# Kernel tuning notes

Hardware: AMD Instinct MI355X
Metric: run time of the kernel (lower is better)

Reference implementation:

```python
import jax, jax.numpy as jnp
import numpy as np

L, H, E, V, BS = 12, 12, 768, 50257, 1024  # layers, heads, n_embd, vocab, block_size
B, T = 2, 1024
D = E // H


def setup_inputs() -> dict:
    key = jax.random.key(0)
    ks = jax.random.split(key, 10)
    s = 0.02
    d = {}
    d["idx"] = jax.random.randint(ks[0], (B, T), 0, V)
    d["targets"] = jax.random.randint(ks[1], (B, T), 0, V)
    # embeddings (wte tied with lm_head)
    d["wte"] = (jax.random.normal(ks[2], (V, E)) * s).astype(jnp.float32)
    d["wpe"] = (jax.random.normal(ks[3], (BS, E)) * s).astype(jnp.float32)
    # stacked per-layer params; Linear weights stored [in, out] (= torch W.T)
    d["ln1_w"] = jnp.ones((L, E), jnp.float32)
    d["ln1_b"] = jnp.zeros((L, E), jnp.float32)
    d["attn_w"] = (jax.random.normal(ks[4], (L, E, 3 * E)) * s).astype(jnp.float32)
    d["attn_b"] = jnp.zeros((L, 3 * E), jnp.float32)
    d["proj_w"] = (jax.random.normal(ks[5], (L, E, E)) * s).astype(jnp.float32)
    d["proj_b"] = jnp.zeros((L, E), jnp.float32)
    d["ln2_w"] = jnp.ones((L, E), jnp.float32)
    d["ln2_b"] = jnp.zeros((L, E), jnp.float32)
    d["fc_w"] = (jax.random.normal(ks[6], (L, E, 4 * E)) * s).astype(jnp.float32)
    d["fc_b"] = jnp.zeros((L, 4 * E), jnp.float32)
    d["fcproj_w"] = (jax.random.normal(ks[7], (L, 4 * E, E)) * s).astype(jnp.float32)
    d["fcproj_b"] = jnp.zeros((L, E), jnp.float32)
    d["lnf_w"] = jnp.ones((E,), jnp.float32)
    d["lnf_b"] = jnp.zeros((E,), jnp.float32)
    return d


def _ln(x, w, b, eps=1e-5):
    m = jnp.mean(x, -1, keepdims=True)
    v = jnp.mean(jnp.square(x - m), -1, keepdims=True)
    return (x - m) * jax.lax.rsqrt(v + eps) * w + b


def _block(x, p, mask):
    l1w, l1b, aw, ab, pw, pb, l2w, l2b, fw, fb, fpw, fpb = p
    Bx, Tx, C = x.shape
    # causal self-attention (explicit QK^T + mask + softmax + AV, as in source)
    qkv = _ln(x, l1w, l1b) @ aw + ab                       # [B,T,3E]
    q, k, v = jnp.split(qkv, 3, axis=-1)
    q = q.reshape(Bx, Tx, H, D).transpose(0, 2, 1, 3)       # [B,H,T,D]
    k = k.reshape(Bx, Tx, H, D).transpose(0, 2, 1, 3)
    v = v.reshape(Bx, Tx, H, D).transpose(0, 2, 1, 3)
    att = jnp.einsum('bhqd,bhkd->bhqk', q, k) * (1.0 / np.sqrt(D))
    att = jnp.where(mask, att, -jnp.inf)
    att = jax.nn.softmax(att, axis=-1)
    y = jnp.einsum('bhqk,bhkd->bhqd', att, v)
    y = y.transpose(0, 2, 1, 3).reshape(Bx, Tx, C)
    x = x + y @ pw + pb
    # MLP with tanh-approx GELU
    h = jax.nn.gelu(_ln(x, l2w, l2b) @ fw + fb, approximate=True)
    x = x + h @ fpw + fpb
    return x


def reference(idx, targets, wte, wpe, ln1_w, ln1_b, attn_w, attn_b, proj_w, proj_b,
              ln2_w, ln2_b, fc_w, fc_b, fcproj_w, fcproj_b, lnf_w, lnf_b):
    Tq = idx.shape[1]
    x = wte[idx] + wpe[:Tq]                                 # [B,T,E]
    mask = jnp.tril(jnp.ones((Tq, Tq), dtype=bool))

    def step(x, p):
        return _block(x, p, mask), None

    layer_params = (ln1_w, ln1_b, attn_w, attn_b, proj_w, proj_b,
                    ln2_w, ln2_b, fc_w, fc_b, fcproj_w, fcproj_b)
    x, _ = jax.lax.scan(step, x, layer_params)
    x = _ln(x, lnf_w, lnf_b)
    logits = x @ wte.T                                      # tied lm_head, [B,T,V]
    logp = jax.nn.log_softmax(logits, axis=-1)
    nll = -jnp.take_along_axis(logp, targets[..., None], axis=-1)[..., 0]
    loss = jnp.mean(nll)
    return logits, loss
```

## Files before the change

### kernel.cpp

```cpp
#include <hip/hip_runtime.h>
#include <hip/hip_bf16.h>
#include <math.h>

#define LNUM 12
#define HNUM 12
#define EDIM 768
#define VDIM 50257
#define BDIM 2
#define TDIM 1024
#define BT (BDIM*TDIM)
#define E3 (3*EDIM)
#define E4 (4*EDIM)
#define NPB (2*((VDIM+127)/128))

typedef __bf16 bf16x8 __attribute__((ext_vector_type(8)));
typedef __bf16 bf16x4 __attribute__((ext_vector_type(4)));
typedef float f32x4 __attribute__((ext_vector_type(4)));

__device__ __forceinline__ float gelu_f(float x) {
    float u = 0.7978845608028654f * (x + 0.044715f * x * x * x);
    return 0.5f * x * (1.0f + tanhf(u));
}

__device__ __forceinline__ void gl16(const void* g, void* l) {
    __builtin_amdgcn_global_load_lds(
        (const __attribute__((address_space(1))) unsigned int*)g,
        (__attribute__((address_space(3))) unsigned int*)l,
        16, 0, 0);
}

__global__ __launch_bounds__(256) void embed_kernel(
    const int* __restrict__ idx, const float* __restrict__ wte,
    const float* __restrict__ wpe, float* __restrict__ x)
{
    const int row = blockIdx.x;
    const int t = row % TDIM;
    const int tok = idx[row];
    const float* we = wte + (size_t)tok * EDIM;
    const float* pe = wpe + (size_t)t * EDIM;
    float* xr = x + (size_t)row * EDIM;
    for (int e = threadIdx.x; e < EDIM; e += 256) xr[e] = we[e] + pe[e];
}

__global__ __launch_bounds__(256) void ln_kernel(
    const float* __restrict__ in, const float* __restrict__ w,
    const float* __restrict__ b, __bf16* __restrict__ out)
{
    const int row = blockIdx.x * 4 + (threadIdx.x >> 6);
    const int lane = threadIdx.x & 63;
    const float4* xr = (const float4*)(in + (size_t)row * EDIM);
    float4 a0 = xr[lane], a1 = xr[64 + lane], a2 = xr[128 + lane];
    float s = a0.x + a0.y + a0.z + a0.w + a1.x + a1.y + a1.z + a1.w
            + a2.x + a2.y + a2.z + a2.w;
    #pragma unroll
    for (int off = 32; off; off >>= 1) s += __shfl_xor(s, off);
    const float mean = s * (1.0f / EDIM);
    float4 d0 = make_float4(a0.x - mean, a0.y - mean, a0.z - mean, a0.w - mean);
    float4 d1 = make_float4(a1.x - mean, a1.y - mean, a1.z - mean, a1.w - mean);
    float4 d2 = make_float4(a2.x - mean, a2.y - mean, a2.z - mean, a2.w - mean);
    float v = d0.x*d0.x + d0.y*d0.y + d0.z*d0.z + d0.w*d0.w
            + d1.x*d1.x + d1.y*d1.y + d1.z*d1.z + d1.w*d1.w
            + d2.x*d2.x + d2.y*d2.y + d2.z*d2.z + d2.w*d2.w;
    #pragma unroll
    for (int off = 32; off; off >>= 1) v += __shfl_xor(v, off);
    const float inv = rsqrtf(v * (1.0f / EDIM) + 1e-5f);
    const float4* w4 = (const float4*)w;
    const float4* b4 = (const float4*)b;
    __bf16* orow = out + (size_t)row * EDIM;
    #pragma unroll
    for (int c = 0; c < 3; ++c) {
        float4 dd = c == 0 ? d0 : (c == 1 ? d1 : d2);
        float4 ww = w4[c * 64 + lane], bb = b4[c * 64 + lane];
        bf16x4 o;
        o[0] = (__bf16)(dd.x * inv * ww.x + bb.x);
        o[1] = (__bf16)(dd.y * inv * ww.y + bb.y);
        o[2] = (__bf16)(dd.z * inv * ww.z + bb.z);
        o[3] = (__bf16)(dd.w * inv * ww.w + bb.w);
        *(bf16x4*)(orow + c * 256 + lane * 4) = o;
    }
}

__global__ __launch_bounds__(256) void convt_kernel(
    const float* __restrict__ in, __bf16* __restrict__ out, int K, int N)
{
    in  += (size_t)blockIdx.z * K * N;
    out += (size_t)blockIdx.z * K * N;
    __shared__ float t[32][33];
    const int n0 = blockIdx.x * 32, k0 = blockIdx.y * 32;
    const int r = threadIdx.x >> 3, c = (threadIdx.x & 7) * 4;
    float4 v = *(const float4*)(in + (size_t)(k0 + r) * N + n0 + c);
    t[r][c + 0] = v.x; t[r][c + 1] = v.y; t[r][c + 2] = v.z; t[r][c + 3] = v.w;
    __syncthreads();
    bf16x4 o;
    o[0] = (__bf16)t[c + 0][r];
    o[1] = (__bf16)t[c + 1][r];
    o[2] = (__bf16)t[c + 2][r];
    o[3] = (__bf16)t[c + 3][r];
    *(bf16x4*)(out + (size_t)(n0 + r) * K + k0 + c) = o;
}

__global__ __launch_bounds__(256) void cvt_kernel(
    const float* __restrict__ in, __bf16* __restrict__ out, long n4)
{
    for (long i = blockIdx.x * 256L + threadIdx.x; i < n4; i += (long)gridDim.x * 256L) {
        float4 v = ((const float4*)in)[i];
        out[i * 4 + 0] = (__bf16)v.x;
        out[i * 4 + 1] = (__bf16)v.y;
        out[i * 4 + 2] = (__bf16)v.z;
        out[i * 4 + 3] = (__bf16)v.w;
    }
}

template<int BM, int BN, int BK, bool BIAS, bool GELU_, bool RES_, bool OUTBF, bool NGUARD, bool LOGITS>
__global__ __launch_bounds__(256, 2) void mgemm(
    const __bf16* __restrict__ A, const __bf16* __restrict__ Bt,
    const float* __restrict__ bias, const float* __restrict__ res,
    void* __restrict__ Cout, float* __restrict__ part, int M, int N, int K)
{
    constexpr int WM = BM / 2, WN = BN / 2;
    constexpr int FM = WM / 16, FN = WN / 16;
    constexpr int KS = BK / 32;
    constexpr int TBA = BM * BK * 2;
    constexpr int TBB = BN * BK * 2;
    constexpr int rA = TBA / 4096, rB = TBB / 4096;
    constexpr int RPI = 2048 / BK;
    constexpr int CPR = BK / 8;
    __shared__ __align__(16) __bf16 As[3 * BM * BK];
    __shared__ __align__(16) __bf16 Bs[3 * BN * BK];
    const int tid = threadIdx.x;
    const int lane = tid & 63;
    const int wave = tid >> 6;
    const int wr = wave >> 1, wc = wave & 1;

    int bm, bn;
    if (LOGITS) {
        const int wg = blockIdx.x;
        bm = (wg >> 3) & 7;
        bn = (wg & 7) + ((wg >> 6) << 3);
        if (bn * BN >= N) return;
    } else { bm = blockIdx.y; bn = blockIdx.x; }
    const int m0 = bm * BM;
    const int n0 = bn * BN;

    const int srow = tid / CPR;
    const int skey = (BK == 32) ? ((srow >> 1) & 3) : (srow & 7);
    const int c0 = (tid % CPR) ^ skey;

    const __bf16* gA = A + (size_t)(m0 + srow) * K + c0 * 8;
    const __bf16* gB[rB];
    #pragma unroll
    for (int r = 0; r < rB; ++r) {
        int nr = n0 + srow + r * RPI;
        if (NGUARD) nr = nr < N ? nr : N - 1;
        gB[r] = Bt + (size_t)nr * K + c0 * 8;
    }

    const int fr = lane & 15;
    const int g = lane >> 4;
    const int fkey = (BK == 32) ? ((fr >> 1) & 3) : (fr & 7);

    f32x4 acc[FM][FN];
    #pragma unroll
    for (int i = 0; i < FM; i++)
        #pragma unroll
        for (int j = 0; j < FN; j++) acc[i][j] = (f32x4){0.f, 0.f, 0.f, 0.f};

    const int nt = K / BK;

    auto stage = [&](int kk, int b) {
        #pragma unroll
        for (int r = 0; r < rA; ++r)
            gl16(gA + (size_t)r * RPI * K + kk, (char*)As + b * TBA + r * 4096 + tid * 16);
        #pragma unroll
        for (int r = 0; r < rB; ++r)
            gl16(gB[r] + kk, (char*)Bs + b * TBB + r * 4096 + tid * 16);
    };

    stage(0, 0);
    if (nt > 1) stage(BK, 1);

    int b0 = 0, b1 = 1, b2 = 2;
    for (int t = 0; t < nt; ++t) {
        if (t + 1 < nt) {
            static_assert(rA + rB == 4 || rA + rB == 6, "vmcnt literal");
            if constexpr (rA + rB == 4) asm volatile("s_waitcnt vmcnt(4)" ::: "memory");
            else                        asm volatile("s_waitcnt vmcnt(6)" ::: "memory");
        } else {
            asm volatile("s_waitcnt vmcnt(0)" ::: "memory");
        }
        asm volatile("s_barrier" ::: "memory");
        if (t + 2 < nt) stage((t + 2) * BK, b2);

        const char* pa = (const char*)As + b0 * TBA;
        const char* pb = (const char*)Bs + b0 * TBB;
        bf16x8 af[FM][KS], bfr[FN][KS];
        #pragma unroll
        for (int i = 0; i < FM; i++)
            #pragma unroll
            for (int kc = 0; kc < KS; kc++)
                af[i][kc] = *(const bf16x8*)(pa + (wr * WM + i * 16 + fr) * (2 * BK)
                                                + (((kc * 4 + g) ^ fkey) << 4));
        #pragma unroll
        for (int j = 0; j < FN; j++)
            #pragma unroll
            for (int kc = 0; kc < KS; kc++)
                bfr[j][kc] = *(const bf16x8*)(pb + (wc * WN + j * 16 + fr) * (2 * BK)
                                                 + (((kc * 4 + g) ^ fkey) << 4));
        #pragma unroll
        for (int kc = 0; kc < KS; kc++)
            #pragma unroll
            for (int i = 0; i < FM; i++)
                #pragma unroll
                for (int j = 0; j < FN; j++)
                    acc[i][j] = __builtin_amdgcn_mfma_f32_16x16x32_bf16(af[i][kc], bfr[j][kc], acc[i][j], 0, 0, 0);
        const int tmp = b0; b0 = b1; b1 = b2; b2 = tmp;
    }

    const int crow = g * 4;
    if constexpr (LOGITS) {
        constexpr int NH = WN / 64;
        const int cg0 = bn * (BN / 64) + wc * NH;
        #pragma unroll
        for (int i = 0; i < FM; i++) {
            #pragma unroll
            for (int r = 0; r < 4; r++) {
                const int m = m0 + wr * WM + i * 16 + crow + r;
                float se[NH];
                #pragma unroll
                for (int h = 0; h < NH; h++) se[h] = 0.f;
                #pragma unroll
                for (int j = 0; j < FN; j++) {
                    const int n = n0 + wc * WN + j * 16 + fr;
                    if (n < N) {
                        float v = acc[i][j][r];
                        ((float*)Cout)[(size_t)m * N + n] = v;
                        se[j >> 2] += __expf(v);
                    }
                }
                #pragma unroll
                for (int h = 0; h < NH; h++) {
                    float sh = se[h];
                    sh += __shfl_xor(sh, 1); sh += __shfl_xor(sh, 2);
                    sh += __shfl_xor(sh, 4); sh += __shfl_xor(sh, 8);
                    if (fr == 0 && (n0 + wc * WN + h * 64) < N)
                        part[(size_t)m * NPB + cg0 + h] = sh;
                }
            }
        }
    } else {
        #pragma unroll
        for (int i = 0; i < FM; i++) {
            #pragma unroll
            for (int r = 0; r < 4; r++) {
                const int m = m0 + wr * WM + i * 16 + crow + r;
                #pragma unroll
                for (int j = 0; j < FN; j++) {
                    const int n = n0 + wc * WN + j * 16 + fr;
                    if (!NGUARD || n < N) {
                        float v = acc[i][j][r];
                        if (BIAS) v += bias[n];
                        if (GELU_) v = gelu_f(v);
                        if (RES_) v += res[(size_t)m * N + n];
                        if (OUTBF) ((__bf16*)Cout)[(size_t)m * N + n] = (__bf16)v;
                        else       ((float*)Cout)[(size_t)m * N + n] = v;
                    }
                }
            }
        }
    }
}

__global__ __launch_bounds__(128) void fattn_kernel(
    const __bf16* __restrict__ qkv, __bf16* __restrict__ y)
{
    const int bq = gridDim.x - 1 - blockIdx.x;
    const int h = blockIdx.y, b = blockIdx.z;
    const int tid = threadIdx.x, lane = tid & 63, w = tid >> 6;
    const int fr = lane & 15, g = lane >> 4;

    __shared__ __align__(16) __bf16 Ks[64 * 64];
    __shared__ __align__(16) __bf16 Vt[64 * 64];
    __shared__ __align__(16) __bf16 Ps[2][16 * 64];

    const __bf16* base = qkv + (size_t)b * TDIM * E3;
    const int q0w = bq * 32 + w * 16;
    const int NT = (bq >> 1) + 1;
    const int last = NT - 1;

    bf16x8 qf[2];
    {
        const __bf16* qp = base + (size_t)(q0w + fr) * E3 + h * 64 + g * 8;
        qf[0] = *(const bf16x8*)qp;
        qf[1] = *(const bf16x8*)(qp + 32);
    }

    const int r0 = tid >> 3, ch = tid & 7;
    bf16x8 kr[4], vr[4];

    #pragma unroll
    for (int it = 0; it < 4; ++it) {
        const int row = it * 16 + r0;
        const __bf16* gp = base + (size_t)row * E3 + EDIM + h * 64 + ch * 8;
        kr[it] = *(const bf16x8*)gp;
        vr[it] = *(const bf16x8*)(gp + EDIM);
    }
    #pragma unroll
    for (int it = 0; it < 4; ++it) {
        const int row = it * 16 + r0;
        *(bf16x8*)(Ks + row * 64 + ((ch ^ (row & 7)) << 3)) = kr[it];
        #pragma unroll
        for (int j = 0; j < 8; ++j) {
            const int d = ch * 8 + j;
            const int key = ((d >> 3) ^ d) & 7;
            Vt[d * 64 + ((((row >> 3) ^ key) << 3) + (row & 7))] = vr[it][j];
        }
    }
    __syncthreads();

    float m[4] = {-1e30f, -1e30f, -1e30f, -1e30f};
    float l[4] = {0.f, 0.f, 0.f, 0.f};
    f32x4 acc[4];
    #pragma unroll
    for (int jd = 0; jd < 4; ++jd) acc[jd] = (f32x4){0.f, 0.f, 0.f, 0.f};

    for (int kt = 0; kt < NT; ++kt) {
        if (kt < last) {
            const int k1 = (kt + 1) * 64;
            #pragma unroll
            for (int it = 0; it < 4; ++it) {
                const int row = it * 16 + r0;
                const __bf16* gp = base + (size_t)(k1 + row) * E3 + EDIM + h * 64 + ch * 8;
                kr[it] = *(const bf16x8*)gp;
                vr[it] = *(const bf16x8*)(gp + EDIM);
            }
        }

        const int k0 = kt * 64;
        f32x4 s[4];
        #pragma unroll
        for (int jf = 0; jf < 4; ++jf) {
            const int krow = jf * 16 + fr;
            f32x4 sv = (f32x4){0.f, 0.f, 0.f, 0.f};
            #pragma unroll
            for (int kc = 0; kc < 2; ++kc) {
                bf16x8 kf = *(const bf16x8*)(Ks + krow * 64 + (((kc * 4 + g) ^ (fr & 7)) << 3));
                sv = __builtin_amdgcn_mfma_f32_16x16x32_bf16(qf[kc], kf, sv, 0, 0, 0);
            }
            s[jf] = sv;
        }
        #pragma unroll
        for (int jf = 0; jf < 4; ++jf)
            #pragma unroll
            for (int r = 0; r < 4; ++r) s[jf][r] *= 0.125f;
        if (kt == last) {
            #pragma unroll
            for (int jf = 0; jf < 4; ++jf) {
                const int k = k0 + jf * 16 + fr;
                #pragma unroll
                for (int r = 0; r < 4; ++r) {
                    const int q = q0w + g * 4 + r;
                    if (k > q) s[jf][r] = -1e30f;
                }
            }
        }

        #pragma unroll
        for (int r = 0; r < 4; ++r) {
            float mx = fmaxf(fmaxf(s[0][r], s[1][r]), fmaxf(s[2][r], s[3][r]));
            mx = fmaxf(mx, __shfl_xor(mx, 1));
            mx = fmaxf(mx, __shfl_xor(mx, 2));
            mx = fmaxf(mx, __shfl_xor(mx, 4));
            mx = fmaxf(mx, __shfl_xor(mx, 8));
            const float mn = fmaxf(m[r], mx);
            const float sc2 = __expf(m[r] - mn);
            m[r] = mn;
            float rs = 0.f;
            #pragma unroll
            for (int jf = 0; jf < 4; ++jf) {
                const float p = __expf(s[jf][r] - mn);
                s[jf][r] = p;
                rs += p;
            }
            rs += __shfl_xor(rs, 1);
            rs += __shfl_xor(rs, 2);
            rs += __shfl_xor(rs, 4);
            rs += __shfl_xor(rs, 8);
            l[r] = l[r] * sc2 + rs;
            #pragma unroll
            for (int jd = 0; jd < 4; ++jd) acc[jd][r] *= sc2;
        }

        __bf16* pw = &Ps[w][0];
        #pragma unroll
        for (int jf = 0; jf < 4; ++jf) {
            const int chp = jf * 2 + (fr >> 3);
            #pragma unroll
            for (int r = 0; r < 4; ++r) {
                const int row = g * 4 + r;
                pw[row * 64 + (((chp ^ (row & 7)) << 3) + (fr & 7))] = (__bf16)s[jf][r];
            }
        }
        asm volatile("s_waitcnt lgkmcnt(0)" ::: "memory");
        bf16x8 pa[2];
        #pragma unroll
        for (int kc = 0; kc < 2; ++kc)
            pa[kc] = *(const bf16x8*)(pw + fr * 64 + (((kc * 4 + g) ^ (fr & 7)) << 3));

        #pragma unroll
        for (int jd = 0; jd < 4; ++jd) {
            const int d = jd * 16 + fr;
            const int key = ((d >> 3) ^ d) & 7;
            #pragma unroll
            for (int kc = 0; kc < 2; ++kc) {
                bf16x8 vf = *(const bf16x8*)(Vt + d * 64 + (((kc * 4 + g) ^ key) << 3));
                acc[jd] = __builtin_amdgcn_mfma_f32_16x16x32_bf16(pa[kc], vf, acc[jd], 0, 0, 0);
            }
        }

        if (kt < last) {
            __syncthreads();
            #pragma unroll
            for (int it = 0; it < 4; ++it) {
                const int row = it * 16 + r0;
                *(bf16x8*)(Ks + row * 64 + ((ch ^ (row & 7)) << 3)) = kr[it];
                #pragma unroll
                for (int j = 0; j < 8; ++j) {
                    const int d = ch * 8 + j;
                    const int key = ((d >> 3) ^ d) & 7;
                    Vt[d * 64 + ((((row >> 3) ^ key) << 3) + (row & 7))] = vr[it][j];
                }
            }
            __syncthreads();
        }
    }

    #pragma unroll
    for (int r = 0; r < 4; ++r) {
        const float inv = 1.0f / l[r];
        const int q = q0w + g * 4 + r;
        __bf16* yp = y + ((size_t)(b * TDIM + q)) * EDIM + h * 64;
        #pragma unroll
        for (int jd = 0; jd < 4; ++jd)
            yp[jd * 16 + fr] = (__bf16)(acc[jd][r] * inv);
    }
}

__global__ __launch_bounds__(256) void lsefin_kernel(
    const float* __restrict__ part, const float* __restrict__ logits,
    const int* __restrict__ targets, float* __restrict__ rr)
{
    const int row = blockIdx.x, tid = threadIdx.x;
    float s = 0.f;
    for (int j = tid; j < NPB; j += 256) s += part[(size_t)row * NPB + j];
    #pragma unroll
    for (int off = 32; off; off >>= 1) s += __shfl_xor(s, off);
    __shared__ float red[4];
    if ((tid & 63) == 0) red[tid >> 6] = s;
    __syncthreads();
    if (tid == 0) {
        float S = red[0] + red[1] + red[2] + red[3];
        rr[row] = logf(S) - logits[(size_t)row * VDIM + targets[row]];
    }
}

__global__ __launch_bounds__(256) void loss_reduce_kernel(
    const float* __restrict__ rr, float* __restrict__ out)
{
    const int tid = threadIdx.x;
    float s = 0.f;
    for (int i = tid; i < BT; i += 256) s += rr[i];
    #pragma unroll
    for (int off = 32; off; off >>= 1) s += __shfl_xor(s, off);
    __shared__ float red[4];
    if ((tid & 63) == 0) red[tid >> 6] = s;
    __syncthreads();
    if (tid == 0) out[0] = (red[0] + red[1] + red[2] + red[3]) * (1.0f / BT);
}

extern "C" void kernel_launch(void* const* d_in, const int* in_sizes, int n_in,
                              void* d_out, int out_size, void* d_ws, size_t ws_size,
                              hipStream_t stream)
{
    const int*   idx     = (const int*)d_in[0];
    const int*   targets = (const int*)d_in[1];
    const float* wte     = (const float*)d_in[2];
    const float* wpe     = (const float*)d_in[3];
    const float* ln1_w   = (const float*)d_in[4];
    const float* ln1_b   = (const float*)d_in[5];
    const float* attn_w  = (const float*)d_in[6];
    const float* attn_b  = (const float*)d_in[7];
    const float* proj_w  = (const float*)d_in[8];
    const float* proj_b  = (const float*)d_in[9];
    const float* ln2_w   = (const float*)d_in[10];
    const float* ln2_b   = (const float*)d_in[11];
    const float* fc_w    = (const float*)d_in[12];
    const float* fc_b    = (const float*)d_in[13];
    const float* fcp_w   = (const float*)d_in[14];
    const float* fcp_b   = (const float*)d_in[15];
    const float* lnf_w   = (const float*)d_in[16];
    const float* lnf_b   = (const float*)d_in[17];

    float* logits = (float*)d_out;

    const size_t slq = (size_t)EDIM * E3, slp = (size_t)EDIM * EDIM;
    const size_t slf = (size_t)EDIM * E4, slfp = (size_t)E4 * EDIM;

    char* wp = (char*)d_ws;
    float*  x     = (float*)wp;   wp += (size_t)BT * EDIM * 4;
    __bf16* qkvb  = (__bf16*)wp;  wp += (size_t)BT * E3 * 2;
    __bf16* xnbf  = (__bf16*)wp;  wp += (size_t)BT * EDIM * 2;
    __bf16* ybf   = (__bf16*)wp;  wp += (size_t)BT * EDIM * 2;
    __bf16* hbf   = (__bf16*)wp;  wp += (size_t)BT * E4 * 2;
    __bf16* wteb  = (__bf16*)wp;  wp += (size_t)VDIM * EDIM * 2;
    float*  part  = (float*)wp;   wp += (size_t)BT * NPB * 4;
    float*  rr    = (float*)wp;   wp += (size_t)BT * 4;
    __bf16* wqkvb = (__bf16*)wp;

    const size_t wbytes_all = (slq + slp + slf + slfp) * 2 * LNUM;
    const size_t used = (size_t)(wp - (char*)d_ws);
    const bool big = ws_size >= used + wbytes_all;
    const size_t L = big ? LNUM : 1;
    __bf16* wprjb = wqkvb + slq * L;
    __bf16* wfcb  = wprjb + slp * L;
    __bf16* wfpb  = wfcb  + slf * L;

    embed_kernel<<<BT, 256, 0, stream>>>(idx, wte, wpe, x);
    cvt_kernel<<<2048, 256, 0, stream>>>(wte, wteb, (long)VDIM * EDIM / 4);

    if (big) {
        convt_kernel<<<dim3(E3 / 32, EDIM / 32, LNUM), 256, 0, stream>>>(attn_w, wqkvb, EDIM, E3);
        convt_kernel<<<dim3(EDIM / 32, EDIM / 32, LNUM), 256, 0, stream>>>(proj_w, wprjb, EDIM, EDIM);
        convt_kernel<<<dim3(E4 / 32, EDIM / 32, LNUM), 256, 0, stream>>>(fc_w, wfcb, EDIM, E4);
        convt_kernel<<<dim3(EDIM / 32, E4 / 32, LNUM), 256, 0, stream>>>(fcp_w, wfpb, E4, EDIM);
    }

    for (int l = 0; l < LNUM; ++l) {
        const __bf16* wq = wqkvb + (big ? (size_t)l * slq : 0);
        const __bf16* wpj = wprjb + (big ? (size_t)l * slp : 0);
        const __bf16* wf = wfcb + (big ? (size_t)l * slf : 0);
        const __bf16* wfp = wfpb + (big ? (size_t)l * slfp : 0);

        ln_kernel<<<BT / 4, 256, 0, stream>>>(x, ln1_w + (size_t)l * EDIM,
                                              ln1_b + (size_t)l * EDIM, xnbf);
        if (!big)
            convt_kernel<<<dim3(E3 / 32, EDIM / 32), 256, 0, stream>>>(
                attn_w + (size_t)l * slq, (__bf16*)wq, EDIM, E3);
        mgemm<64, 64, 64, true, false, false, true, false, false>
            <<<dim3(E3 / 64, BT / 64), 256, 0, stream>>>(
            xnbf, wq, attn_b + (size_t)l * E3, nullptr, qkvb, nullptr, BT, E3, EDIM);
        fattn_kernel<<<dim3(TDIM / 32, HNUM, BDIM), 128, 0, stream>>>(qkvb, ybf);
        if (!big)
            convt_kernel<<<dim3(EDIM / 32, EDIM / 32), 256, 0, stream>>>(
                proj_w + (size_t)l * slp, (__bf16*)wpj, EDIM, EDIM);
        mgemm<64, 64, 64, true, false, true, false, false, false>
            <<<dim3(EDIM / 64, BT / 64), 256, 0, stream>>>(
            ybf, wpj, proj_b + (size_t)l * EDIM, x, x, nullptr, BT, EDIM, EDIM);
        ln_kernel<<<BT / 4, 256, 0, stream>>>(x, ln2_w + (size_t)l * EDIM,
                                              ln2_b + (size_t)l * EDIM, xnbf);
        if (!big)
            convt_kernel<<<dim3(E4 / 32, EDIM / 32), 256, 0, stream>>>(
                fc_w + (size_t)l * slf, (__bf16*)wf, EDIM, E4);
        mgemm<64, 64, 64, true, true, false, true, false, false>
            <<<dim3(E4 / 64, BT / 64), 256, 0, stream>>>(
            xnbf, wf, fc_b + (size_t)l * E4, nullptr, hbf, nullptr, BT, E4, EDIM);
        if (!big)
            convt_kernel<<<dim3(EDIM / 32, E4 / 32), 256, 0, stream>>>(
                fcp_w + (size_t)l * slfp, (__bf16*)wfp, E4, EDIM);
        mgemm<64, 64, 64, true, false, true, false, false, false>
            <<<dim3(EDIM / 64, BT / 64), 256, 0, stream>>>(
            hbf, wfp, fcp_b + (size_t)l * EDIM, x, x, nullptr, BT, EDIM, E4);
    }

    ln_kernel<<<BT / 4, 256, 0, stream>>>(x, lnf_w, lnf_b, xnbf);
    mgemm<256, 128, 32, false, false, false, false, true, true>
        <<<dim3(64 * 50), 256, 0, stream>>>(
        xnbf, wteb, nullptr, nullptr, logits, part, BT, VDIM, EDIM);
    lsefin_kernel<<<BT, 256, 0, stream>>>(part, logits, targets, rr);
    loss_reduce_kernel<<<1, 256, 0, stream>>>(rr, logits + (size_t)BT * VDIM);
}
```

Before: 2.139 ms.

## Split-K the projection GEMMs and fuse residual reduction with next LayerNorm

The two N=768 GEMMs (attention proj and MLP down-proj) now run as 2-way split-K launches that write fp32 partial sums. A new redln kernel adds both partials, the bias and the residual, updates x, and applies the following LayerNorm in one pass, so the separate LN launches go away. Attention MFMA sections are also wrapped in s_setprio raises. This gives the small-grid GEMMs more blocks to fill the GPU, at the cost of writing and reading an extra 2xBTxE fp32 partial buffer each time.

```diff
diff --git a/kernel.cpp b/kernel.cpp
--- a/kernel.cpp
+++ b/kernel.cpp
@@ -76,6 +76,55 @@
         o[1] = (__bf16)(dd.y * inv * ww.y + bb.y);
         o[2] = (__bf16)(dd.z * inv * ww.z + bb.z);
         o[3] = (__bf16)(dd.w * inv * ww.w + bb.w);
+        *(bf16x4*)(orow + c * 256 + lane * 4) = o;
+    }
+}
+
+__global__ __launch_bounds__(256) void redln_kernel(
+    const float* __restrict__ ps, const float* __restrict__ bias,
+    float* __restrict__ x, const float* __restrict__ w,
+    const float* __restrict__ b, __bf16* __restrict__ out)
+{
+    const int row = blockIdx.x * 4 + (threadIdx.x >> 6);
+    const int lane = threadIdx.x & 63;
+    const float4* p0 = (const float4*)(ps + (size_t)row * EDIM);
+    const float4* p1 = (const float4*)(ps + (size_t)(BT + row) * EDIM);
+    float4* xr = (float4*)(x + (size_t)row * EDIM);
+    const float4* b4 = (const float4*)bias;
+    float4 a[3];
+    #pragma unroll
+    for (int c = 0; c < 3; ++c) {
+        const int i = c * 64 + lane;
+        float4 u = p0[i], v = p1[i], xx = xr[i], bb = b4[i];
+        a[c] = make_float4(u.x + v.x + xx.x + bb.x, u.y + v.y + xx.y + bb.y,
+                           u.z + v.z + xx.z + bb.z, u.w + v.w + xx.w + bb.w);
+        xr[i] = a[c];
+    }
+    float s = a[0].x + a[0].y + a[0].z + a[0].w + a[1].x + a[1].y + a[1].z + a[1].w
+            + a[2].x + a[2].y + a[2].z + a[2].w;
+    #pragma unroll
+    for (int off = 32; off; off >>= 1) s += __shfl_xor(s, off);
+    const float mean = s * (1.0f / EDIM);
+    float v = 0.f;
+    #pragma unroll
+    for (int c = 0; c < 3; ++c) {
+        a[c] = make_float4(a[c].x - mean, a[c].y - mean, a[c].z - mean, a[c].w - mean);
+        v += a[c].x * a[c].x + a[c].y * a[c].y + a[c].z * a[c].z + a[c].w * a[c].w;
+    }
+    #pragma unroll
+    for (int off = 32; off; off >>= 1) v += __shfl_xor(v, off);
+    const float inv = rsqrtf(v * (1.0f / EDIM) + 1e-5f);
+    const float4* w4 = (const float4*)w;
+    const float4* lb4 = (const float4*)b;
+    __bf16* orow = out + (size_t)row * EDIM;
+    #pragma unroll
+    for (int c = 0; c < 3; ++c) {
+        float4 ww = w4[c * 64 + lane], bb = lb4[c * 64 + lane];
+        bf16x4 o;
+        o[0] = (__bf16)(a[c].x * inv * ww.x + bb.x);
+        o[1] = (__bf16)(a[c].y * inv * ww.y + bb.y);
+        o[2] = (__bf16)(a[c].z * inv * ww.z + bb.z);
+        o[3] = (__bf16)(a[c].w * inv * ww.w + bb.w);
         *(bf16x4*)(orow + c * 256 + lane * 4) = o;
     }
 }
@@ -115,7 +164,7 @@
 __global__ __launch_bounds__(256, 2) void mgemm(
     const __bf16* __restrict__ A, const __bf16* __restrict__ Bt,
     const float* __restrict__ bias, const float* __restrict__ res,
-    void* __restrict__ Cout, float* __restrict__ part, int M, int N, int K)
+    void* __restrict__ Cout, float* __restrict__ part, int M, int N, int K, int lda)
 {
     constexpr int WM = BM / 2, WN = BN / 2;
     constexpr int FM = WM / 16, FN = WN / 16;
@@ -141,18 +190,20 @@
     } else { bm = blockIdx.y; bn = blockIdx.x; }
     const int m0 = bm * BM;
     const int n0 = bn * BN;
+    const int kbase = blockIdx.z * K;
+    const size_t zoff = (size_t)blockIdx.z * M * N;
 
     const int srow = tid / CPR;
     const int skey = (BK == 32) ? ((srow >> 1) & 3) : (srow & 7);
     const int c0 = (tid % CPR) ^ skey;
 
-    const __bf16* gA = A + (size_t)(m0 + srow) * K + c0 * 8;
+    const __bf16* gA = A + (size_t)(m0 + srow) * lda + kbase + c0 * 8;
     const __bf16* gB[rB];
     #pragma unroll
     for (int r = 0; r < rB; ++r) {
         int nr = n0 + srow + r * RPI;
         if (NGUARD) nr = nr < N ? nr : N - 1;
-        gB[r] = Bt + (size_t)nr * K + c0 * 8;
+        gB[r] = Bt + (size_t)nr * lda + kbase + c0 * 8;
     }
 
     const int fr = lane & 15;
@@ -170,7 +221,7 @@
     auto stage = [&](int kk, int b) {
         #pragma unroll
         for (int r = 0; r < rA; ++r)
-            gl16(gA + (size_t)r * RPI * K + kk, (char*)As + b * TBA + r * 4096 + tid * 16);
+            gl16(gA + (size_t)r * RPI * lda + kk, (char*)As + b * TBA + r * 4096 + tid * 16);
         #pragma unroll
         for (int r = 0; r < rB; ++r)
             gl16(gB[r] + kk, (char*)Bs + b * TBB + r * 4096 + tid * 16);
@@ -261,8 +312,8 @@
                         if (BIAS) v += bias[n];
                         if (GELU_) v = gelu_f(v);
                         if (RES_) v += res[(size_t)m * N + n];
-                        if (OUTBF) ((__bf16*)Cout)[(size_t)m * N + n] = (__bf16)v;
-                        else       ((float*)Cout)[(size_t)m * N + n] = v;
+                        if (OUTBF) ((__bf16*)Cout)[zoff + (size_t)m * N + n] = (__bf16)v;
+                        else       ((float*)Cout)[zoff + (size_t)m * N + n] = v;
                     }
                 }
             }
@@ -337,6 +388,7 @@
 
         const int k0 = kt * 64;
         f32x4 s[4];
+        __builtin_amdgcn_s_setprio(1);
         #pragma unroll
         for (int jf = 0; jf < 4; ++jf) {
             const int krow = jf * 16 + fr;
@@ -348,6 +400,7 @@
             }
             s[jf] = sv;
         }
+        __builtin_amdgcn_s_setprio(0);
         #pragma unroll
         for (int jf = 0; jf < 4; ++jf)
             #pragma unroll
@@ -406,6 +459,7 @@
         for (int kc = 0; kc < 2; ++kc)
             pa[kc] = *(const bf16x8*)(pw + fr * 64 + (((kc * 4 + g) ^ (fr & 7)) << 3));
 
+        __builtin_amdgcn_s_setprio(1);
         #pragma unroll
         for (int jd = 0; jd < 4; ++jd) {
             const int d = jd * 16 + fr;
@@ -416,6 +470,7 @@
                 acc[jd] = __builtin_amdgcn_mfma_f32_16x16x32_bf16(pa[kc], vf, acc[jd], 0, 0, 0);
             }
         }
+        __builtin_amdgcn_s_setprio(0);
 
         if (kt < last) {
             __syncthreads();
@@ -513,6 +568,7 @@
     __bf16* hbf   = (__bf16*)wp;  wp += (size_t)BT * E4 * 2;
     __bf16* wteb  = (__bf16*)wp;  wp += (size_t)VDIM * EDIM * 2;
     float*  part  = (float*)wp;   wp += (size_t)BT * NPB * 4;
+    float*  psum  = (float*)wp;   wp += (size_t)2 * BT * EDIM * 4;
     float*  rr    = (float*)wp;   wp += (size_t)BT * 4;
     __bf16* wqkvb = (__bf16*)wp;
 
@@ -534,47 +590,51 @@
         convt_kernel<<<dim3(EDIM / 32, E4 / 32, LNUM), 256, 0, stream>>>(fcp_w, wfpb, E4, EDIM);
     }
 
+    ln_kernel<<<BT / 4, 256, 0, stream>>>(x, ln1_w, ln1_b, xnbf);
+
     for (int l = 0; l < LNUM; ++l) {
         const __bf16* wq = wqkvb + (big ? (size_t)l * slq : 0);
         const __bf16* wpj = wprjb + (big ? (size_t)l * slp : 0);
         const __bf16* wf = wfcb + (big ? (size_t)l * slf : 0);
         const __bf16* wfp = wfpb + (big ? (size_t)l * slfp : 0);
 
-        ln_kernel<<<BT / 4, 256, 0, stream>>>(x, ln1_w + (size_t)l * EDIM,
-                                              ln1_b + (size_t)l * EDIM, xnbf);
         if (!big)
             convt_kernel<<<dim3(E3 / 32, EDIM / 32), 256, 0, stream>>>(
                 attn_w + (size_t)l * slq, (__bf16*)wq, EDIM, E3);
         mgemm<64, 64, 64, true, false, false, true, false, false>
             <<<dim3(E3 / 64, BT / 64), 256, 0, stream>>>(
-            xnbf, wq, attn_b + (size_t)l * E3, nullptr, qkvb, nullptr, BT, E3, EDIM);
+            xnbf, wq, attn_b + (size_t)l * E3, nullptr, qkvb, nullptr, BT, E3, EDIM, EDIM);
         fattn_kernel<<<dim3(TDIM / 32, HNUM, BDIM), 128, 0, stream>>>(qkvb, ybf);
         if (!big)
             convt_kernel<<<dim3(EDIM / 32, EDIM / 32), 256, 0, stream>>>(
                 proj_w + (size_t)l * slp, (__bf16*)wpj, EDIM, EDIM);
-        mgemm<64, 64, 64, true, false, true, false, false, false>
-            <<<dim3(EDIM / 64, BT / 64), 256, 0, stream>>>(
-            ybf, wpj, proj_b + (size_t)l * EDIM, x, x, nullptr, BT, EDIM, EDIM);
-        ln_kernel<<<BT / 4, 256, 0, stream>>>(x, ln2_w + (size_t)l * EDIM,
-                                              ln2_b + (size_t)l * EDIM, xnbf);
+        mgemm<64, 64, 64, false, false, false, false, false, false>
+            <<<dim3(EDIM / 64, BT / 64, 2), 256, 0, stream>>>(
+            ybf, wpj, nullptr, nullptr, psum, nullptr, BT, EDIM, EDIM / 2, EDIM);
+        redln_kernel<<<BT / 4, 256, 0, stream>>>(
+            psum, proj_b + (size_t)l * EDIM, x,
+            ln2_w + (size_t)l * EDIM, ln2_b + (size_t)l * EDIM, xnbf);
         if (!big)
             convt_kernel<<<dim3(E4 / 32, EDIM / 32), 256, 0, stream>>>(
                 fc_w + (size_t)l * slf, (__bf16*)wf, EDIM, E4);
         mgemm<64, 64, 64, true, true, false, true, false, false>
             <<<dim3(E4 / 64, BT / 64), 256, 0, stream>>>(
-            xnbf, wf, fc_b + (size_t)l * E4, nullptr, hbf, nullptr, BT, E4, EDIM);
+            xnbf, wf, fc_b + (size_t)l * E4, nullptr, hbf, nullptr, BT, E4, EDIM, EDIM);
         if (!big)
             convt_kernel<<<dim3(EDIM / 32, E4 / 32), 256, 0, stream>>>(
                 fcp_w + (size_t)l * slfp, (__bf16*)wfp, E4, EDIM);
-        mgemm<64, 64, 64, true, false, true, false, false, false>
-            <<<dim3(EDIM / 64, BT / 64), 256, 0, stream>>>(
-            hbf, wfp, fcp_b + (size_t)l * EDIM, x, x, nullptr, BT, EDIM, E4);
-    }
-
-    ln_kernel<<<BT / 4, 256, 0, stream>>>(x, lnf_w, lnf_b, xnbf);
+        mgemm<64, 64, 64, false, false, false, false, false, false>
+            <<<dim3(EDIM / 64, BT / 64, 2), 256, 0, stream>>>(
+            hbf, wfp, nullptr, nullptr, psum, nullptr, BT, EDIM, E4 / 2, E4);
+        const float* nw = (l + 1 < LNUM) ? ln1_w + (size_t)(l + 1) * EDIM : lnf_w;
+        const float* nb = (l + 1 < LNUM) ? ln1_b + (size_t)(l + 1) * EDIM : lnf_b;
+        redln_kernel<<<BT / 4, 256, 0, stream>>>(
+            psum, fcp_b + (size_t)l * EDIM, x, nw, nb, xnbf);
+    }
+
     mgemm<256, 128, 32, false, false, false, false, true, true>
         <<<dim3(64 * 50), 256, 0, stream>>>(
-        xnbf, wteb, nullptr, nullptr, logits, part, BT, VDIM, EDIM);
+        xnbf, wteb, nullptr, nullptr, logits, part, BT, VDIM, EDIM, EDIM);
     lsefin_kernel<<<BT, 256, 0, stream>>>(part, logits, targets, rr);
     loss_reduce_kernel<<<1, 256, 0, stream>>>(rr, logits + (size_t)BT * VDIM);
 }
```

New measurement: 2.016 ms. 1.06x faster.
